# Performance work log

Measured on AMD Instinct MI355X. Metric: run time of the kernel, lower is better.

The kernel has to match this reference:

```python
import jax, jax.numpy as jnp
import numpy as np

N = 20000
E = 640000
D = 128
NORM_FACTOR = 100.0
LN_EPS = 1e-5


def _layer_norm(x, g, b):
    mu = jnp.mean(x, axis=-1, keepdims=True)
    var = jnp.var(x, axis=-1, keepdims=True)
    return (x - mu) * jax.lax.rsqrt(var + LN_EPS) * g + b


def setup_inputs() -> dict:
    key = jax.random.key(0)
    ks = jax.random.split(key, 16)

    def lin(k, fan_in, shape):
        bound = 1.0 / np.sqrt(fan_in)
        return jax.random.uniform(k, shape, jnp.float32, -bound, bound)

    h = jax.random.normal(ks[0], (N, D), jnp.float32)
    distances = jax.random.uniform(ks[1], (E, 1), jnp.float32)
    edges = jax.random.randint(ks[2], (2, E), 0, N, jnp.int64)
    node_mask = jnp.ones((N, 1), jnp.float32)
    edge_mask = jnp.ones((E, 1), jnp.float32)

    return {
        "h": h, "distances": distances, "node_mask": node_mask, "edge_mask": edge_mask,
        # linear: in->out
        "lin_w": lin(ks[3], D, (D, D)), "lin_b": lin(ks[4], D, (D,)),
        # att_mlp: (2D+1)->2D -> 2D->D -> D->1
        "att_w1": lin(ks[5], 2 * D + 1, (2 * D, 2 * D + 1)), "att_b1": lin(ks[5], 2 * D + 1, (2 * D,)),
        "att_w2": lin(ks[6], 2 * D, (D, 2 * D)), "att_b2": lin(ks[6], 2 * D, (D,)),
        "att_w3": lin(ks[7], D, (1, D)), "att_b3": lin(ks[7], D, (1,)),
        # node_mlp: D->D, LN, SiLU, D->D
        "nm_w1": lin(ks[8], D, (D, D)), "nm_b1": lin(ks[8], D, (D,)),
        "nm_ln_g": jnp.ones((D,), jnp.float32), "nm_ln_b": jnp.zeros((D,), jnp.float32),
        "nm_w2": lin(ks[9], D, (D, D)), "nm_b2": lin(ks[9], D, (D,)),
        # final LayerNorm
        "ln_g": jnp.ones((D,), jnp.float32), "ln_b": jnp.zeros((D,), jnp.float32),
        "edges": edges,
    }


def reference(h, distances, node_mask, edge_mask,
              lin_w, lin_b, att_w1, att_b1, att_w2, att_b2, att_w3, att_b3,
              nm_w1, nm_b1, nm_ln_g, nm_ln_b, nm_w2, nm_b2, ln_g, ln_b, edges):
    x = h @ lin_w.T + lin_b                                  # [N, D]
    row, col = edges[0], edges[1]
    x_row = x[row]                                           # [E, D]
    x_col = x[col]                                           # [E, D]

    # DenseAtt
    d = distances * edge_mask
    x_cat = jnp.concatenate([x_row, x_col, d], axis=1)       # [E, 2D+1]
    a = jax.nn.silu(x_cat @ att_w1.T + att_b1)
    a = jax.nn.silu(a @ att_w2.T + att_b2)
    att = jax.nn.sigmoid(a @ att_w3.T + att_b3) * edge_mask  # [E, 1]

    agg = x_col * att                                        # [E, D]
    out = jax.ops.segment_sum(agg, row, num_segments=N) / NORM_FACTOR

    # node_mlp + residual
    o = out @ nm_w1.T + nm_b1
    o = jax.nn.silu(_layer_norm(o, nm_ln_g, nm_ln_b))
    o = o @ nm_w2.T + nm_b2
    hh = o + x

    hh = _layer_norm(hh, ln_g, ln_b)
    hh = jax.nn.silu(hh)                                     # act = SiLU
    return hh
```

## Files before the change

### kernel.cpp

```cpp
#include <hip/hip_runtime.h>
#include <hip/hip_bf16.h>

#define N_NODES 20000
#define E_EDGES 640000
#define DIM 128
#define CAP 96
#define EPB 64
#define NPB 8
#define XST 264

typedef __attribute__((ext_vector_type(8))) short bf16x8;
typedef __attribute__((ext_vector_type(4))) float f32x4;

#define LOG2E 1.44269504f
__device__ __forceinline__ float fsilu(float x) {
    return x * __builtin_amdgcn_rcpf(1.f + __builtin_amdgcn_exp2f(-LOG2E * x));
}
__device__ __forceinline__ float fsig(float x) {
    return __builtin_amdgcn_rcpf(1.f + __builtin_amdgcn_exp2f(-LOG2E * x));
}

__device__ __forceinline__ unsigned short f2bf(float x) {
    union { float f; unsigned u; } v; v.f = x;
    unsigned r = (v.u + 0x7fffu + ((v.u >> 16) & 1u)) >> 16;
    return (unsigned short)r;
}
__device__ __forceinline__ float bf2f(unsigned short s) {
    union { unsigned u; float f; } v; v.u = ((unsigned)s) << 16;
    return v.f;
}
__device__ __forceinline__ unsigned pack_bf16(float lo, float hi) {
    union { float f; unsigned u; } a, b; a.f = lo; b.f = hi;
    unsigned ul = a.u + 0x8000u, uh = b.u + 0x8000u;
    return __builtin_amdgcn_perm(uh, ul, 0x07060302u);
}

#define PRE_PREP_BLOCKS 64
#define PRE_LIN_BLOCKS  625
#define PRE_ADJ_BLOCKS  2500
__global__ __launch_bounds__(256) void pre_kernel(
    const float* __restrict__ w1, const float* __restrict__ w2,
    unsigned short* __restrict__ w1b, float* __restrict__ w1p,
    unsigned short* __restrict__ w2b,
    const float* __restrict__ h, const float* __restrict__ lw,
    const float* __restrict__ lb, float* __restrict__ x,
    unsigned short* __restrict__ xb,
    const int* __restrict__ edges, int* __restrict__ cnt,
    int2* __restrict__ adj2, int E) {
    __shared__ float hs[32][128];
    int b = blockIdx.x;
    int t = threadIdx.x;

    if (b < PRE_PREP_BLOCKS) {
        int i = b * 256 + t;
        const int stride = PRE_PREP_BLOCKS * 256;
        for (int idx = i; idx < 256 * 256; idx += stride) {
            int o = idx >> 8, k = idx & 255;
            w1b[idx] = f2bf(w1[o * 257 + k]);
        }
        for (int idx = i; idx < 128 * 256; idx += stride) {
            int n2 = idx >> 8, p = idx & 255;
            int bb = p & ~31, off = p & 31;
            int ksrc = bb + (off >> 1) + ((off & 1) << 4);
            w2b[idx] = f2bf(w2[n2 * 256 + ksrc]);
        }
        for (int idx = i; idx < 256; idx += stride) {
            int bb = idx & ~31, off = idx & 31;
            int ksrc = bb + (off >> 1) + ((off & 1) << 4);
            w1p[idx] = w1[ksrc * 257 + 256];
        }
    } else if (b < PRE_PREP_BLOCKS + PRE_LIN_BLOCKS) {
        int nb = b - PRE_PREP_BLOCKS;
        int n0 = nb * 32;
        int ch = t & 127, g = t >> 7;
#pragma unroll
        for (int j = 0; j < 16; ++j) hs[g * 16 + j][ch] = h[(size_t)(n0 + g * 16 + j) * DIM + ch];
        __syncthreads();
        float acc[16];
#pragma unroll
        for (int j = 0; j < 16; ++j) acc[j] = 0.f;
        for (int kc = 0; kc < 128; kc += 4) {
            float4 wv = *(const float4*)&lw[(size_t)ch * DIM + kc];
#pragma unroll
            for (int j = 0; j < 16; ++j)
                acc[j] += wv.x * hs[g * 16 + j][kc] + wv.y * hs[g * 16 + j][kc + 1]
                        + wv.z * hs[g * 16 + j][kc + 2] + wv.w * hs[g * 16 + j][kc + 3];
        }
        float bias = lb[ch];
#pragma unroll
        for (int j = 0; j < 16; ++j) {
            float v = acc[j] + bias;
            int n = n0 + g * 16 + j;
            x[(size_t)n * DIM + ch] = v;
            xb[(size_t)n * DIM + ch] = f2bf(v);
        }
    } else {
        int e = (b - PRE_PREP_BLOCKS - PRE_LIN_BLOCKS) * 256 + t;
        if (e < E) {
            int r = edges[e];
            int col = edges[E + e];
            int slot = atomicAdd(&cnt[r], 1);
            if (slot < CAP) { int2 v; v.x = e; v.y = col; adj2[(size_t)r * CAP + slot] = v; }
        }
    }
}

__global__ __launch_bounds__(1024) void scan_kernel(const int* __restrict__ cnt,
                                                    int* __restrict__ off) {
    __shared__ int part[1024];
    int t = threadIdx.x;
    int base = t * 20;
    int loc[20];
    int s = 0;
#pragma unroll
    for (int i = 0; i < 20; ++i) {
        int idx = base + i;
        int v = 0;
        if (idx < N_NODES) { v = cnt[idx]; v = v > CAP ? CAP : v; }
        loc[i] = s; s += v;
    }
    part[t] = s;
    __syncthreads();
    int run = s;
    for (int d = 1; d < 1024; d <<= 1) {
        int v = (t >= d) ? part[t - d] : 0;
        __syncthreads();
        part[t] += v;
        __syncthreads();
    }
    int ex = part[t] - run;
#pragma unroll
    for (int i = 0; i < 20; ++i) {
        int idx = base + i;
        if (idx < N_NODES) off[idx] = ex + loc[i];
    }
    if (t == 1023) off[N_NODES] = part[1023];
}

#define MID_PRC_BLOCKS 1250
#define MID_FLAT_BLOCKS 2500
__global__ __launch_bounds__(256) void mid_kernel(
    const unsigned short* __restrict__ xb,
    const unsigned short* __restrict__ w1b,
    const float* __restrict__ b1,
    unsigned short* __restrict__ prb, unsigned short* __restrict__ pcb,
    const int2* __restrict__ adj2, const int* __restrict__ cnt,
    const int* __restrict__ off,
    const float* __restrict__ dist, const float* __restrict__ emask,
    int4* __restrict__ flat) {
    int b = blockIdx.x;
    if (b < MID_PRC_BLOCKS) {
        int n0 = b * 16;
        int w = threadIdx.x >> 6, lane = threadIdx.x & 63;
        int lrow = lane & 15, quad = lane >> 4;

        bf16x8 a[4];
#pragma unroll
        for (int kk = 0; kk < 4; ++kk)
            a[kk] = *(const bf16x8*)&xb[(size_t)(n0 + lrow) * DIM + kk * 32 + quad * 8];

        f32x4 z = {0.f, 0.f, 0.f, 0.f};
#pragma unroll
        for (int i = 0; i < 8; ++i) {
            int gt = w * 8 + i;
            int half = gt >> 4;
            int obase = (gt & 15) * 16;
            f32x4 acc = z;
#pragma unroll
            for (int kk = 0; kk < 4; ++kk) {
                bf16x8 bfrag = *(const bf16x8*)&w1b[(size_t)(obase + lrow) * 256 + half * 128 + kk * 32 + quad * 8];
                acc = __builtin_amdgcn_mfma_f32_16x16x32_bf16(a[kk], bfrag, acc, 0, 0, 0);
            }
            int o = obase + lrow;
            if (half == 0) {
                float bias = b1[o];
#pragma unroll
                for (int r = 0; r < 4; ++r)
                    prb[(size_t)(n0 + quad * 4 + r) * 256 + o] = f2bf(acc[r] + bias);
            } else {
#pragma unroll
                for (int r = 0; r < 4; ++r)
                    pcb[(size_t)(n0 + quad * 4 + r) * 256 + o] = f2bf(acc[r]);
            }
        }
    } else {
        int fb = b - MID_PRC_BLOCKS;
        int n0 = fb * NPB;
        int jg = threadIdx.x >> 5, l = threadIdx.x & 31;
        int n = n0 + jg;
        int c = cnt[n]; c = c > CAP ? CAP : c;
        int o = off[n];
        const int2* al = adj2 + (size_t)n * CAP;
        for (int i = l; i < c; i += 32) {
            int2 v = al[i];
            float em = emask[v.x];
            float dv = dist[v.x] * em;
            int4 wv;
            union { float f; int i; } u1, u2; u1.f = dv; u2.f = em;
            wv.x = n; wv.y = v.y; wv.z = u1.i; wv.w = u2.i;
            flat[o + i] = wv;
        }
    }
}

__global__ __launch_bounds__(512, 4) void edge_kernel(
    const unsigned short* __restrict__ prb, const unsigned short* __restrict__ pcb,
    const int4* __restrict__ flat, const int* __restrict__ off,
    const float* __restrict__ w1p,
    const unsigned short* __restrict__ w2b, const float* __restrict__ b2,
    const float* __restrict__ w3, const float* __restrict__ b3v,
    float* __restrict__ attv) {
    __shared__ unsigned short buf[EPB * XST];
    __shared__ float part[8][EPB];
    __shared__ float w1ps[256];
    __shared__ float dvals[EPB], emv[EPB];
    __shared__ int ridx[EPB], cidx[EPB];

    int tid = threadIdx.x;
    int eb = blockIdx.x * EPB;

    if (tid < EPB) {
        int count = off[N_NODES];
        int idx = eb + tid;
        int4 v;
        if (idx < count) v = flat[idx];
        else { v.x = 0; v.y = 0; v.z = 0; v.w = 0; }
        ridx[tid] = v.x; cidx[tid] = v.y;
        union { int i; float f; } a, bu; a.i = v.z; bu.i = v.w;
        dvals[tid] = a.f; emv[tid] = bu.f;
    }
    if (tid >= 64 && tid < 320) w1ps[tid - 64] = w1p[tid - 64];

    int wave = tid >> 6, lane = tid & 63;
    int lrow = lane & 15, quad = lane >> 4;
    int n2 = wave * 16 + lrow;
    float bias2 = b2[n2];
    float w3v = w3[n2];

    __syncthreads();

    {
        int ge = tid >> 3, cb = tid & 7;
        const unsigned short* prow = prb + (size_t)ridx[ge] * 256 + cb * 32;
        const unsigned short* pcp  = pcb + (size_t)cidx[ge] * 256 + cb * 32;
        float d = dvals[ge];
        unsigned* wrow = (unsigned*)&buf[ge * XST + cb * 32];
        const float* wp = &w1ps[cb * 32];

        bf16x8 pA = *(const bf16x8*)&prow[0];
        bf16x8 pB = *(const bf16x8*)&prow[16];
        bf16x8 qA = *(const bf16x8*)&pcp[0];
        bf16x8 qB = *(const bf16x8*)&pcp[16];
#pragma unroll
        for (int l = 0; l < 8; ++l) {
            float s0 = bf2f((unsigned short)pA[l]) + bf2f((unsigned short)qA[l]) + d * wp[2 * l];
            float s1 = bf2f((unsigned short)pB[l]) + bf2f((unsigned short)qB[l]) + d * wp[2 * l + 1];
            wrow[l] = pack_bf16(fsilu(s0), fsilu(s1));
        }
        pA = *(const bf16x8*)&prow[8];
        pB = *(const bf16x8*)&prow[24];
        qA = *(const bf16x8*)&pcp[8];
        qB = *(const bf16x8*)&pcp[24];
#pragma unroll
        for (int l = 0; l < 8; ++l) {
            float s0 = bf2f((unsigned short)pA[l]) + bf2f((unsigned short)qA[l]) + d * wp[16 + 2 * l];
            float s1 = bf2f((unsigned short)pB[l]) + bf2f((unsigned short)qB[l]) + d * wp[16 + 2 * l + 1];
            wrow[8 + l] = pack_bf16(fsilu(s0), fsilu(s1));
        }
    }
    __syncthreads();

    f32x4 zz = {0.f, 0.f, 0.f, 0.f};
    f32x4 acc2[4];
#pragma unroll
    for (int mt = 0; mt < 4; ++mt) acc2[mt] = zz;

    for (int kk = 0; kk < 8; ++kk) {
        int ka = kk * 32 + quad * 8;
        bf16x8 bfrag = *(const bf16x8*)&w2b[(size_t)n2 * 256 + ka];
#pragma unroll
        for (int mt = 0; mt < 4; ++mt) {
            bf16x8 a = *(bf16x8*)&buf[(mt * 16 + lrow) * XST + ka];
            acc2[mt] = __builtin_amdgcn_mfma_f32_16x16x32_bf16(a, bfrag, acc2[mt], 0, 0, 0);
        }
    }

    float s[4][4];
#pragma unroll
    for (int mt = 0; mt < 4; ++mt)
#pragma unroll
        for (int r = 0; r < 4; ++r)
            s[mt][r] = fsilu(acc2[mt][r] + bias2) * w3v;
#pragma unroll
    for (int off2 = 1; off2 < 16; off2 <<= 1) {
#pragma unroll
        for (int mt = 0; mt < 4; ++mt)
#pragma unroll
            for (int r = 0; r < 4; ++r)
                s[mt][r] += __shfl_xor(s[mt][r], off2);
    }
    if (lrow == 0) {
#pragma unroll
        for (int mt = 0; mt < 4; ++mt)
#pragma unroll
            for (int r = 0; r < 4; ++r)
                part[wave][mt * 16 + quad * 4 + r] = s[mt][r];
    }
    __syncthreads();

    if (tid < EPB) {
        float ssum = b3v[0];
#pragma unroll
        for (int w = 0; w < 8; ++w) ssum += part[w][tid];
        attv[eb + tid] = fsig(ssum) * emv[tid];
    }
}

__global__ __launch_bounds__(256) void node_kernel(
    const float* __restrict__ attv, const int2* __restrict__ adj2,
    const int* __restrict__ cnt, const int* __restrict__ off,
    const unsigned short* __restrict__ xb,
    const float* __restrict__ x,
    const float* __restrict__ w1, const float* __restrict__ bb1,
    const float* __restrict__ lng, const float* __restrict__ lnb,
    const float* __restrict__ w2, const float* __restrict__ bb2,
    const float* __restrict__ gF, const float* __restrict__ bF,
    float* __restrict__ out, int E) {
    __shared__ float atts[NPB][CAP];
    __shared__ int   cols[NPB][CAP];
    __shared__ float outv[NPB][128];
    __shared__ float bufs[NPB][128];
    __shared__ float mu_s[NPB], rs_s[NPB];
    __shared__ int cnts[NPB];

    int t = threadIdx.x;
    int n0 = blockIdx.x * NPB;

    if (t < NPB) { int c = cnt[n0 + t]; cnts[t] = c > CAP ? CAP : c; }
    __syncthreads();

    {
        int jg = t >> 5, l = t & 31;
        int c = cnts[jg];
        const int2* al = adj2 + (size_t)(n0 + jg) * CAP;
        const float* av = attv + off[n0 + jg];
        for (int i = l; i < c; i += 32) {
            atts[jg][i] = av[i];
            cols[jg][i] = al[i].y;
        }
    }
    __syncthreads();

    int w = t >> 6, lane = t & 63;
#pragma unroll
    for (int jj = 0; jj < 2; ++jj) {
        int j = w * 2 + jj;
        int c = cnts[j];
        float lo0 = 0.f, hi0 = 0.f, lo1 = 0.f, hi1 = 0.f;
        float lo2 = 0.f, hi2 = 0.f, lo3 = 0.f, hi3 = 0.f;
        int i = 0;
        for (; i + 3 < c; i += 4) {
            unsigned u0 = *(const unsigned*)&xb[(size_t)cols[j][i]     * DIM + lane * 2];
            unsigned u1 = *(const unsigned*)&xb[(size_t)cols[j][i + 1] * DIM + lane * 2];
            unsigned u2 = *(const unsigned*)&xb[(size_t)cols[j][i + 2] * DIM + lane * 2];
            unsigned u3 = *(const unsigned*)&xb[(size_t)cols[j][i + 3] * DIM + lane * 2];
            float w0 = atts[j][i], w1v = atts[j][i + 1], w2v = atts[j][i + 2], w3v = atts[j][i + 3];
            lo0 += w0 * bf2f((unsigned short)(u0 & 0xffff)); hi0 += w0 * bf2f((unsigned short)(u0 >> 16));
            lo1 += w1v * bf2f((unsigned short)(u1 & 0xffff)); hi1 += w1v * bf2f((unsigned short)(u1 >> 16));
            lo2 += w2v * bf2f((unsigned short)(u2 & 0xffff)); hi2 += w2v * bf2f((unsigned short)(u2 >> 16));
            lo3 += w3v * bf2f((unsigned short)(u3 & 0xffff)); hi3 += w3v * bf2f((unsigned short)(u3 >> 16));
        }
        for (; i < c; ++i) {
            unsigned u0 = *(const unsigned*)&xb[(size_t)cols[j][i] * DIM + lane * 2];
            float w0 = atts[j][i];
            lo0 += w0 * bf2f((unsigned short)(u0 & 0xffff));
            hi0 += w0 * bf2f((unsigned short)(u0 >> 16));
        }
        outv[j][lane * 2]     = ((lo0 + lo1) + (lo2 + lo3)) * 0.01f;
        outv[j][lane * 2 + 1] = ((hi0 + hi1) + (hi2 + hi3)) * 0.01f;
    }
    __syncthreads();

    int h = t >> 7, ch = t & 127;
    float xres[4];
#pragma unroll
    for (int jj = 0; jj < 4; ++jj)
        xres[jj] = x[(size_t)(n0 + h * 4 + jj) * DIM + ch];

    float a1[4] = {0, 0, 0, 0};
    for (int kc = 0; kc < 128; kc += 4) {
        float4 wv = *(const float4*)&w1[(size_t)ch * DIM + kc];
#pragma unroll
        for (int jj = 0; jj < 4; ++jj) {
            int j = h * 4 + jj;
            float4 ov = *(const float4*)&outv[j][kc];
            a1[jj] += wv.x * ov.x + wv.y * ov.y + wv.z * ov.z + wv.w * ov.w;
        }
    }
    float bias1 = bb1[ch];
#pragma unroll
    for (int jj = 0; jj < 4; ++jj) bufs[h * 4 + jj][ch] = a1[jj] + bias1;
    __syncthreads();

    {
        int j = t >> 5, l = t & 31;
        float s = 0.f, qq = 0.f;
#pragma unroll
        for (int i = 0; i < 4; ++i) { float v = bufs[j][l + 32 * i]; s += v; qq += v * v; }
#pragma unroll
        for (int off2 = 16; off2; off2 >>= 1) { s += __shfl_xor(s, off2); qq += __shfl_xor(qq, off2); }
        if (l == 0) {
            float mu = s * (1.f / 128.f);
            float var = qq * (1.f / 128.f) - mu * mu;
            mu_s[j] = mu; rs_s[j] = __builtin_amdgcn_rsqf(var + 1e-5f);
        }
    }
    __syncthreads();

    float g = lng[ch], bb = lnb[ch];
    float h2[4];
#pragma unroll
    for (int jj = 0; jj < 4; ++jj) {
        int j = h * 4 + jj;
        h2[jj] = fsilu((bufs[j][ch] - mu_s[j]) * rs_s[j] * g + bb);
    }
    __syncthreads();
#pragma unroll
    for (int jj = 0; jj < 4; ++jj) bufs[h * 4 + jj][ch] = h2[jj];
    __syncthreads();

    float a3[4] = {0, 0, 0, 0};
    for (int kc = 0; kc < 128; kc += 4) {
        float4 wv = *(const float4*)&w2[(size_t)ch * DIM + kc];
#pragma unroll
        for (int jj = 0; jj < 4; ++jj) {
            int j = h * 4 + jj;
            float4 bv = *(const float4*)&bufs[j][kc];
            a3[jj] += wv.x * bv.x + wv.y * bv.y + wv.z * bv.z + wv.w * bv.w;
        }
    }
    float bias2 = bb2[ch];
    float hh[4];
#pragma unroll
    for (int jj = 0; jj < 4; ++jj) hh[jj] = a3[jj] + bias2 + xres[jj];
    __syncthreads();
#pragma unroll
    for (int jj = 0; jj < 4; ++jj) bufs[h * 4 + jj][ch] = hh[jj];
    __syncthreads();

    {
        int j = t >> 5, l = t & 31;
        float s = 0.f, qq = 0.f;
#pragma unroll
        for (int i = 0; i < 4; ++i) { float v = bufs[j][l + 32 * i]; s += v; qq += v * v; }
#pragma unroll
        for (int off2 = 16; off2; off2 >>= 1) { s += __shfl_xor(s, off2); qq += __shfl_xor(qq, off2); }
        if (l == 0) {
            float mu = s * (1.f / 128.f);
            float var = qq * (1.f / 128.f) - mu * mu;
            mu_s[j] = mu; rs_s[j] = __builtin_amdgcn_rsqf(var + 1e-5f);
        }
    }
    __syncthreads();

    float gf = gF[ch], bf = bF[ch];
#pragma unroll
    for (int jj = 0; jj < 4; ++jj) {
        int j = h * 4 + jj;
        float y = (hh[jj] - mu_s[j]) * rs_s[j] * gf + bf;
        out[(size_t)(n0 + j) * DIM + ch] = fsilu(y);
    }
}

extern "C" void kernel_launch(void* const* d_in, const int* in_sizes, int n_in,
                              void* d_out, int out_size, void* d_ws, size_t ws_size,
                              hipStream_t stream) {
    const float* h         = (const float*)d_in[0];
    const float* distances = (const float*)d_in[1];
    const float* edge_mask = (const float*)d_in[3];
    const float* lin_w     = (const float*)d_in[4];
    const float* lin_b     = (const float*)d_in[5];
    const float* att_w1    = (const float*)d_in[6];
    const float* att_b1    = (const float*)d_in[7];
    const float* att_w2    = (const float*)d_in[8];
    const float* att_b2    = (const float*)d_in[9];
    const float* att_w3    = (const float*)d_in[10];
    const float* att_b3    = (const float*)d_in[11];
    const float* nm_w1     = (const float*)d_in[12];
    const float* nm_b1     = (const float*)d_in[13];
    const float* nm_ln_g   = (const float*)d_in[14];
    const float* nm_ln_b   = (const float*)d_in[15];
    const float* nm_w2     = (const float*)d_in[16];
    const float* nm_b2     = (const float*)d_in[17];
    const float* ln_g      = (const float*)d_in[18];
    const float* ln_b      = (const float*)d_in[19];
    const int*   edges     = (const int*)d_in[20];
    float* out = (float*)d_out;

    const int N = N_NODES, E = E_EDGES;

    char* ws = (char*)d_ws;
    float* x            = (float*)ws;            ws += (size_t)N * DIM * 4;
    unsigned short* xb  = (unsigned short*)ws;   ws += (size_t)N * DIM * 2;
    int* cnt            = (int*)ws;              ws += (size_t)N * 4;
    int* off            = (int*)ws;              ws += (size_t)(N + 4) * 4;
    int2* adj2          = (int2*)ws;             ws += (size_t)N * CAP * 8;
    float* attv         = (float*)ws;            ws += (size_t)E * 4;
    unsigned short* w1b = (unsigned short*)ws;   ws += 256 * 256 * 2;
    float* w1p          = (float*)ws;            ws += 256 * 4;
    unsigned short* w2b = (unsigned short*)ws;   ws += 128 * 256 * 2;
    unsigned short* prb = (unsigned short*)ws;   ws += (size_t)N * 256 * 2;
    unsigned short* pcb = (unsigned short*)ws;   ws += (size_t)N * 256 * 2;
    int4* flat          = (int4*)ws;             ws += (size_t)E * 16;

    hipMemsetAsync(cnt, 0, (size_t)N * 4, stream);

    pre_kernel<<<PRE_PREP_BLOCKS + PRE_LIN_BLOCKS + PRE_ADJ_BLOCKS, 256, 0, stream>>>(
        att_w1, att_w2, w1b, w1p, w2b,
        h, lin_w, lin_b, x, xb,
        edges, cnt, adj2, E);
    scan_kernel<<<1, 1024, 0, stream>>>(cnt, off);
    mid_kernel<<<MID_PRC_BLOCKS + MID_FLAT_BLOCKS, 256, 0, stream>>>(
        xb, w1b, att_b1, prb, pcb, adj2, cnt, off, distances, edge_mask, flat);
    edge_kernel<<<E / EPB, 512, 0, stream>>>(prb, pcb, flat, off,
                                             w1p, w2b, att_b2,
                                             att_w3, att_b3, attv);
    node_kernel<<<N / NPB, 256, 0, stream>>>(attv, adj2, cnt, off, xb, x,
                                             nm_w1, nm_b1, nm_ln_g, nm_ln_b,
                                             nm_w2, nm_b2, ln_g, ln_b, out, E);
}
```

Measured before the change: 425.9 us.

## Split adjacency into column and distance arrays, wave-shuffle scan, vectorize LDS stores

The edge-bucketing pass now reads distance and edge mask coalesced in edge order and stores them alongside the column index in separate per-slot arrays. This removes the random gathers of dist/emask by edge id in the flatten pass and lets the node kernel read 4-byte column entries instead of int2. The single-block scan uses wavefront shuffles instead of a barrier-heavy shared-memory Hillis-Steele loop. The edge kernel also buffers packed bf16 activations in registers and writes them to LDS as 16-byte vectors instead of 4-byte stores. The cost is an extra scattered 8-byte write per edge in the pre kernel.

```diff
diff --git a/kernel.cpp b/kernel.cpp
--- a/kernel.cpp
+++ b/kernel.cpp
@@ -11,6 +11,7 @@
 
 typedef __attribute__((ext_vector_type(8))) short bf16x8;
 typedef __attribute__((ext_vector_type(4))) float f32x4;
+typedef __attribute__((ext_vector_type(4))) unsigned u32x4;
 
 #define LOG2E 1.44269504f
 __device__ __forceinline__ float fsilu(float x) {
@@ -45,8 +46,10 @@
     const float* __restrict__ h, const float* __restrict__ lw,
     const float* __restrict__ lb, float* __restrict__ x,
     unsigned short* __restrict__ xb,
-    const int* __restrict__ edges, int* __restrict__ cnt,
-    int2* __restrict__ adj2, int E) {
+    const int* __restrict__ edges,
+    const float* __restrict__ dist, const float* __restrict__ emask,
+    int* __restrict__ cnt,
+    int* __restrict__ adjc, float2* __restrict__ dm, int E) {
     __shared__ float hs[32][128];
     int b = blockIdx.x;
     int t = threadIdx.x;
@@ -99,16 +102,23 @@
         if (e < E) {
             int r = edges[e];
             int col = edges[E + e];
+            float em = emask[e];
+            float dv = dist[e] * em;
             int slot = atomicAdd(&cnt[r], 1);
-            if (slot < CAP) { int2 v; v.x = e; v.y = col; adj2[(size_t)r * CAP + slot] = v; }
+            if (slot < CAP) {
+                adjc[(size_t)r * CAP + slot] = col;
+                float2 de; de.x = dv; de.y = em;
+                dm[(size_t)r * CAP + slot] = de;
+            }
         }
     }
 }
 
 __global__ __launch_bounds__(1024) void scan_kernel(const int* __restrict__ cnt,
                                                     int* __restrict__ off) {
-    __shared__ int part[1024];
+    __shared__ int wsum[16], wbase[16];
     int t = threadIdx.x;
+    int lane = t & 63, wid = t >> 6;
     int base = t * 20;
     int loc[20];
     int s = 0;
@@ -119,22 +129,32 @@
         if (idx < N_NODES) { v = cnt[idx]; v = v > CAP ? CAP : v; }
         loc[i] = s; s += v;
     }
-    part[t] = s;
-    __syncthreads();
-    int run = s;
-    for (int d = 1; d < 1024; d <<= 1) {
-        int v = (t >= d) ? part[t - d] : 0;
-        __syncthreads();
-        part[t] += v;
-        __syncthreads();
-    }
-    int ex = part[t] - run;
+    int inc = s;
+#pragma unroll
+    for (int d = 1; d < 64; d <<= 1) {
+        int u = __shfl_up(inc, d);
+        if (lane >= d) inc += u;
+    }
+    if (lane == 63) wsum[wid] = inc;
+    __syncthreads();
+    if (t < 16) {
+        int v = wsum[t];
+        int inc2 = v;
+#pragma unroll
+        for (int d = 1; d < 16; d <<= 1) {
+            int u = __shfl_up(inc2, d);
+            if (t >= d) inc2 += u;
+        }
+        wbase[t] = inc2 - v;
+        if (t == 15) off[N_NODES] = inc2;
+    }
+    __syncthreads();
+    int ex = wbase[wid] + inc - s;
 #pragma unroll
     for (int i = 0; i < 20; ++i) {
         int idx = base + i;
         if (idx < N_NODES) off[idx] = ex + loc[i];
     }
-    if (t == 1023) off[N_NODES] = part[1023];
 }
 
 #define MID_PRC_BLOCKS 1250
@@ -144,9 +164,8 @@
     const unsigned short* __restrict__ w1b,
     const float* __restrict__ b1,
     unsigned short* __restrict__ prb, unsigned short* __restrict__ pcb,
-    const int2* __restrict__ adj2, const int* __restrict__ cnt,
-    const int* __restrict__ off,
-    const float* __restrict__ dist, const float* __restrict__ emask,
+    const int* __restrict__ adjc, const float2* __restrict__ dm,
+    const int* __restrict__ cnt, const int* __restrict__ off,
     int4* __restrict__ flat) {
     int b = blockIdx.x;
     if (b < MID_PRC_BLOCKS) {
@@ -190,14 +209,13 @@
         int n = n0 + jg;
         int c = cnt[n]; c = c > CAP ? CAP : c;
         int o = off[n];
-        const int2* al = adj2 + (size_t)n * CAP;
+        const int* al = adjc + (size_t)n * CAP;
+        const float2* dl = dm + (size_t)n * CAP;
         for (int i = l; i < c; i += 32) {
-            int2 v = al[i];
-            float em = emask[v.x];
-            float dv = dist[v.x] * em;
+            float2 de = dl[i];
             int4 wv;
-            union { float f; int i; } u1, u2; u1.f = dv; u2.f = em;
-            wv.x = n; wv.y = v.y; wv.z = u1.i; wv.w = u2.i;
+            union { float f; int i; } u1, u2; u1.f = de.x; u2.f = de.y;
+            wv.x = n; wv.y = al[i]; wv.z = u1.i; wv.w = u2.i;
             flat[o + i] = wv;
         }
     }
@@ -244,8 +262,8 @@
         const unsigned short* prow = prb + (size_t)ridx[ge] * 256 + cb * 32;
         const unsigned short* pcp  = pcb + (size_t)cidx[ge] * 256 + cb * 32;
         float d = dvals[ge];
-        unsigned* wrow = (unsigned*)&buf[ge * XST + cb * 32];
         const float* wp = &w1ps[cb * 32];
+        unsigned u[16];
 
         bf16x8 pA = *(const bf16x8*)&prow[0];
         bf16x8 pB = *(const bf16x8*)&prow[16];
@@ -255,7 +273,7 @@
         for (int l = 0; l < 8; ++l) {
             float s0 = bf2f((unsigned short)pA[l]) + bf2f((unsigned short)qA[l]) + d * wp[2 * l];
             float s1 = bf2f((unsigned short)pB[l]) + bf2f((unsigned short)qB[l]) + d * wp[2 * l + 1];
-            wrow[l] = pack_bf16(fsilu(s0), fsilu(s1));
+            u[l] = pack_bf16(fsilu(s0), fsilu(s1));
         }
         pA = *(const bf16x8*)&prow[8];
         pB = *(const bf16x8*)&prow[24];
@@ -265,8 +283,14 @@
         for (int l = 0; l < 8; ++l) {
             float s0 = bf2f((unsigned short)pA[l]) + bf2f((unsigned short)qA[l]) + d * wp[16 + 2 * l];
             float s1 = bf2f((unsigned short)pB[l]) + bf2f((unsigned short)qB[l]) + d * wp[16 + 2 * l + 1];
-            wrow[8 + l] = pack_bf16(fsilu(s0), fsilu(s1));
-        }
+            u[8 + l] = pack_bf16(fsilu(s0), fsilu(s1));
+        }
+        u32x4* w4 = (u32x4*)&buf[ge * XST + cb * 32];
+        u32x4 v0 = {u[0], u[1], u[2], u[3]};
+        u32x4 v1 = {u[4], u[5], u[6], u[7]};
+        u32x4 v2 = {u[8], u[9], u[10], u[11]};
+        u32x4 v3 = {u[12], u[13], u[14], u[15]};
+        w4[0] = v0; w4[1] = v1; w4[2] = v2; w4[3] = v3;
     }
     __syncthreads();
 
@@ -317,7 +341,7 @@
 }
 
 __global__ __launch_bounds__(256) void node_kernel(
-    const float* __restrict__ attv, const int2* __restrict__ adj2,
+    const float* __restrict__ attv, const int* __restrict__ adjc,
     const int* __restrict__ cnt, const int* __restrict__ off,
     const unsigned short* __restrict__ xb,
     const float* __restrict__ x,
@@ -342,11 +366,11 @@
     {
         int jg = t >> 5, l = t & 31;
         int c = cnts[jg];
-        const int2* al = adj2 + (size_t)(n0 + jg) * CAP;
+        const int* al = adjc + (size_t)(n0 + jg) * CAP;
         const float* av = attv + off[n0 + jg];
         for (int i = l; i < c; i += 32) {
             atts[jg][i] = av[i];
-            cols[jg][i] = al[i].y;
+            cols[jg][i] = al[i];
         }
     }
     __syncthreads();
@@ -504,7 +528,8 @@
     unsigned short* xb  = (unsigned short*)ws;   ws += (size_t)N * DIM * 2;
     int* cnt            = (int*)ws;              ws += (size_t)N * 4;
     int* off            = (int*)ws;              ws += (size_t)(N + 4) * 4;
-    int2* adj2          = (int2*)ws;             ws += (size_t)N * CAP * 8;
+    int* adjc           = (int*)ws;              ws += (size_t)N * CAP * 4;
+    float2* dm          = (float2*)ws;           ws += (size_t)N * CAP * 8;
     float* attv         = (float*)ws;            ws += (size_t)E * 4;
     unsigned short* w1b = (unsigned short*)ws;   ws += 256 * 256 * 2;
     float* w1p          = (float*)ws;            ws += 256 * 4;
@@ -518,14 +543,14 @@
     pre_kernel<<<PRE_PREP_BLOCKS + PRE_LIN_BLOCKS + PRE_ADJ_BLOCKS, 256, 0, stream>>>(
         att_w1, att_w2, w1b, w1p, w2b,
         h, lin_w, lin_b, x, xb,
-        edges, cnt, adj2, E);
+        edges, distances, edge_mask, cnt, adjc, dm, E);
     scan_kernel<<<1, 1024, 0, stream>>>(cnt, off);
     mid_kernel<<<MID_PRC_BLOCKS + MID_FLAT_BLOCKS, 256, 0, stream>>>(
-        xb, w1b, att_b1, prb, pcb, adj2, cnt, off, distances, edge_mask, flat);
+        xb, w1b, att_b1, prb, pcb, adjc, dm, cnt, off, flat);
     edge_kernel<<<E / EPB, 512, 0, stream>>>(prb, pcb, flat, off,
                                              w1p, w2b, att_b2,
                                              att_w3, att_b3, attv);
-    node_kernel<<<N / NPB, 256, 0, stream>>>(attv, adj2, cnt, off, xb, x,
+    node_kernel<<<N / NPB, 256, 0, stream>>>(attv, adjc, cnt, off, xb, x,
                                              nm_w1, nm_b1, nm_ln_g, nm_ln_b,
                                              nm_w2, nm_b2, ln_g, ln_b, out, E);
 }
```

New measurement: 413.9 us. -2.8%, faster.
